# Optimization experiments

Hardware: AMD Instinct MI355X
Metric: run time of the kernel (lower is better)

Reference implementation:

```python
import jax, jax.numpy as jnp
import numpy as np
from jax import lax

S_IN = 16; V_IN = 16; S_OUT = 16; V_OUT = 16
SIZE = 7; STRIDE = 2; PAD = 3; EPS = 1e-5
# n_basis per (rep_out, rep_in) pair = n_radial(3) * number of allowed CG paths
NB = {('s','s'): 3, ('s','v'): 3, ('s','t'): 9, ('v','s'): 3, ('v','v'): 9, ('v','t'): 21}
DIMS = {'s': 1, 'v': 3, 't': 9}  # repr1, repr3, repr3x3 dimensions


def _basis(key, nb, d_out, d_in):
    # Stand-in for the constant steerable basis (spherical harmonics x Clebsch-Gordan
    # x radial windows). These are data-independent constants in se3cnn; the compute
    # pattern (weighted basis sum -> dense 3D conv) is identical.
    return jax.random.normal(key, (nb, d_out, d_in, SIZE, SIZE, SIZE), jnp.float32) / np.sqrt(SIZE ** 3)


def setup_inputs() -> dict:
    key = jax.random.key(0)
    ks = jax.random.split(key, 16)
    inp = {"sv": jax.random.normal(ks[0], (4, S_IN + 3 * V_IN, 32, 32, 32), jnp.float32)}
    mul_in = {'s': S_IN, 'v': V_IN, 't': V_IN}
    i = 1
    for o in ['s', 'v']:
        mo = S_OUT if o == 's' else V_OUT
        for a in ['s', 'v', 't']:
            nb = NB[(o, a)]
            inp[f"basis_{o}{a}"] = _basis(ks[i], nb, DIMS[o], DIMS[a])
            inp[f"w_{o}{a}"] = jax.random.normal(ks[i + 1], (mo, mul_in[a], nb), jnp.float32) / np.sqrt(nb * mul_in[a] * DIMS[a])
            i += 2
    inp["bn_g_s"] = jnp.ones((S_OUT,), jnp.float32)
    inp["bn_g_v"] = jnp.ones((V_OUT,), jnp.float32)
    inp["bias_s"] = jnp.zeros((S_OUT,), jnp.float32)
    return inp


def _block(w, basis):
    # w: [mul_out, mul_in, nb], basis: [nb, d_out, d_in, 7,7,7] -> [mul_out*d_out, mul_in*d_in, 7,7,7]
    mo, mi, nb = w.shape
    do, di = basis.shape[1], basis.shape[2]
    k = jnp.einsum('uvb,bijxyz->uivjxyz', w, basis)
    return k.reshape(mo * do, mi * di, SIZE, SIZE, SIZE)


def _forward(sv, w_ss, w_sv, w_st, w_vs, w_vv, w_vt,
             basis_ss, basis_sv, basis_st, basis_vs, basis_vv, basis_vt,
             bn_g_s, bn_g_v, bias_s):
    B = sv.shape[0]; sp = sv.shape[2:]
    # TensorProduct: vector fields -> vector (x) vector = repr3x3 (9 channels each)
    v = sv[:, S_IN:].reshape(B, V_IN, 3, *sp)
    t = jnp.einsum('buixyz,bujxyz->buijxyz', v, v).reshape(B, V_IN * 9, *sp)
    svt = jnp.concatenate([sv, t], axis=1)  # [B, S_IN + 3*V_IN + 9*V_IN, X,Y,Z]
    # SE3Convolution: assemble kernel from steerable basis, then dense 3D conv
    row_s = jnp.concatenate([_block(w_ss, basis_ss), _block(w_sv, basis_sv), _block(w_st, basis_st)], axis=1)
    row_v = jnp.concatenate([_block(w_vs, basis_vs), _block(w_vv, basis_vv), _block(w_vt, basis_vt)], axis=1)
    kernel = jnp.concatenate([row_s, row_v], axis=0)  # [S_OUT + 3*V_OUT, 208, 7,7,7]
    y = lax.conv_general_dilated(svt, kernel, (STRIDE,) * 3, [(PAD, PAD)] * 3,
                                 dimension_numbers=('NCDHW', 'OIDHW', 'NCDHW'))
    osp = y.shape[2:]
    # SE3BatchNorm: per-field second-moment normalization (training-mode batch stats)
    ys = y[:, :S_OUT]
    yv = y[:, S_OUT:].reshape(B, V_OUT, 3, *osp)
    var_s = jnp.mean(ys * ys, axis=(0, 2, 3, 4))
    ys = ys * (bn_g_s / jnp.sqrt(var_s + EPS))[None, :, None, None, None]
    var_v = jnp.mean(yv * yv, axis=(0, 2, 3, 4, 5))
    yv = yv * (bn_g_v / jnp.sqrt(var_v + EPS))[None, :, None, None, None, None]
    # BiasRelu: bias + relu on scalar fields only; vector fields pass through
    ys = jax.nn.relu(ys + bias_s[None, :, None, None, None])
    return jnp.concatenate([ys, yv.reshape(B, 3 * V_OUT, *osp)], axis=1)


def reference(sv, w_ss, w_sv, w_st, w_vs, w_vv, w_vt,
              basis_ss, basis_sv, basis_st, basis_vs, basis_vv, basis_vt,
              bn_g_s, bn_g_v, bias_s):
    return _forward(sv, w_ss, w_sv, w_st, w_vs, w_vv, w_vt,
                    basis_ss, basis_sv, basis_st, basis_vs, basis_vv, basis_vt,
                    bn_g_s, bn_g_v, bias_s)
```

## Files before the change

kernel.cpp:

```cpp
#include <hip/hip_runtime.h>
#include <hip/hip_bf16.h>


using f4  = __attribute__((ext_vector_type(4)))  float;
using f16v= __attribute__((ext_vector_type(16))) float;
using s8  = __attribute__((ext_vector_type(8)))  short;

#define C_TOT 160
#define PZ_   37
#define NTAP  343
#define NROW  (4 * PZ_ * PZ_)
#define KSN   8
#define SLICE_E 1048576

#define AROW    1232
#define AE_ROWS 19
#define AO_ROWS 18
#define AE_SZ   23552
#define AO_OFF  23552
#define AO_SZ   22528
#define B_OFF   46080
#define BSZ     14336
#define LDS_SZ  (B_OFF + 2 * BSZ)

__device__ __forceinline__ void gl_lds16(const void* g, void* l) {
    __builtin_amdgcn_global_load_lds(
        (const __attribute__((address_space(1))) unsigned int*)g,
        (__attribute__((address_space(3))) unsigned int*)l, 16, 0, 0);
}

__device__ __forceinline__ void pair_ij(int p, int& i, int& j) {
    if (p < 3)      { i = p; j = p; }
    else if (p == 3){ i = 0; j = 1; }
    else if (p == 4){ i = 0; j = 2; }
    else            { i = 1; j = 2; }
}

struct bf2 { __hip_bfloat16 x, y; };
struct bh4 { __hip_bfloat16 x, y, z, w; };

__global__ void prep_kernel(
    const float* __restrict__ sv,
    const float* __restrict__ b_ss, const float* __restrict__ w_ss,
    const float* __restrict__ b_sv, const float* __restrict__ w_sv,
    const float* __restrict__ b_st, const float* __restrict__ w_st,
    const float* __restrict__ b_vs, const float* __restrict__ w_vs,
    const float* __restrict__ b_vv, const float* __restrict__ w_vv,
    const float* __restrict__ b_vt, const float* __restrict__ w_vt,
    __hip_bfloat16* __restrict__ xt, __hip_bfloat16* __restrict__ wl)
{
    __shared__ float S[13056];
    const int tid = threadIdx.x;

    if (blockIdx.x < 1372) {
        float* L = S;
        float* W = S + 768;
        const int tap = blockIdx.x >> 2;
        const int jq  = (blockIdx.x & 3) * 10;
        for (int r = tid; r < 750; r += 256) {
            float v;
            if (r < 3)        v = b_ss[r * NTAP + tap];
            else if (r < 12)  v = b_sv[(r - 3) * NTAP + tap];
            else if (r < 93)  v = b_st[(r - 12) * NTAP + tap];
            else if (r < 102) v = b_vs[(r - 93) * NTAP + tap];
            else if (r < 183) v = b_vv[(r - 102) * NTAP + tap];
            else              v = b_vt[(r - 183) * NTAP + tap];
            L[r] = v;
        }
        for (int r = tid; r < 12288; r += 256) {
            float v;
            if (r < 768)       v = w_ss[r];
            else if (r < 1536) v = w_sv[r - 768];
            else if (r < 3840) v = w_st[r - 1536];
            else if (r < 4608) v = w_vs[r - 3840];
            else if (r < 6912) v = w_vv[r - 4608];
            else               v = w_vt[r - 6912];
            W[r] = v;
        }
        __syncthreads();
        for (int j = jq; j < jq + 10; ++j) {
            const int idx = j * 256 + tid;
            const int c = idx % C_TOT, n = idx / C_TOT;
            float acc = 0.f;
            if (n < 16) {
                const int u = n;
                if (c < 16) {
                    for (int t = 0; t < 3; ++t) acc += W[(u*16 + c)*3 + t] * L[t];
                } else if (c < 64) {
                    int mm = (c-16)/3, di = (c-16)%3;
                    for (int t = 0; t < 3; ++t)
                        acc += W[768 + (u*16+mm)*3 + t] * L[3 + t*3 + di];
                } else {
                    int q = c-64, mm = q/6, p = q%6, i, jj;
                    pair_ij(p, i, jj);
                    int d1 = i*3+jj, d2 = jj*3+i;
                    for (int t = 0; t < 9; ++t) {
                        float bs = L[12 + t*9 + d1];
                        if (i != jj) bs += L[12 + t*9 + d2];
                        acc += W[1536 + (u*16+mm)*9 + t] * bs;
                    }
                }
            } else {
                const int u = (n-16)/3, dn = (n-16)%3;
                if (c < 16) {
                    for (int t = 0; t < 3; ++t)
                        acc += W[3840 + (u*16+c)*3 + t] * L[93 + t*3 + dn];
                } else if (c < 64) {
                    int mm = (c-16)/3, di = (c-16)%3;
                    for (int t = 0; t < 9; ++t)
                        acc += W[4608 + (u*16+mm)*9 + t] * L[102 + (t*3+dn)*3 + di];
                } else {
                    int q = c-64, mm = q/6, p = q%6, i, jj;
                    pair_ij(p, i, jj);
                    int d1 = i*3+jj, d2 = jj*3+i;
                    for (int t = 0; t < 21; ++t) {
                        float bs = L[183 + (t*3+dn)*9 + d1];
                        if (i != jj) bs += L[183 + (t*3+dn)*9 + d2];
                        acc += W[6912 + (u*16+mm)*21 + t] * bs;
                    }
                }
            }
            const int chunk = c >> 4, cw = c & 15;
            wl[((size_t)chunk * NTAP + tap) * 1024 + (size_t)n * 16 + cw] =
                __float2bfloat16(acc);
        }
    } else {
        float* row = S;
        const int bid = blockIdx.x - 1372;
        const int y = bid % 37, z = (bid / 37) % 37, b = bid / 1369;
        const bool interior = (z >= 3 && z < 35 && y >= 3 && y < 35);
        if (interior) {
            const float* src = sv + (size_t)b * 2097152 + (z-3) * 1024 + (y-3) * 32;
            for (int f = tid; f < 2048; f += 256) {
                int ch = f >> 5, x = f & 31;
                row[x * 66 + ch] = src[(size_t)ch * 32768 + x];
            }
        }
        __syncthreads();
        for (int e2 = tid; e2 < 38 * 80; e2 += 256) {
            const int s = e2 / 80, cp = e2 % 80, c = cp * 2;
            float v0 = 0.f, v1 = 0.f;
            if (interior && s >= 3 && s < 35) {
                const int x = s - 3;
                if (c < 64) {
                    v0 = row[x * 66 + c];
                    v1 = row[x * 66 + c + 1];
                } else {
                    int q = c - 64, u = q / 6, p = q % 6, i, j;
                    pair_ij(p, i, j);
                    v0 = row[x * 66 + 16 + u * 3 + i] * row[x * 66 + 16 + u * 3 + j];
                    pair_ij(p + 1, i, j);
                    v1 = row[x * 66 + 16 + u * 3 + i] * row[x * 66 + 16 + u * 3 + j];
                }
            }
            bf2 w{__float2bfloat16(v0), __float2bfloat16(v1)};
            const int chunk = c >> 4, cw = c & 15;
            *(bf2*)(xt + ((size_t)chunk * NROW + bid) * 608 + s * 16 + cw) = w;
        }
    }
}

__global__ __launch_bounds__(256, 2) void conv_mfma_kernel(
    const __hip_bfloat16* __restrict__ xt,
    const __hip_bfloat16* __restrict__ wl,
    __hip_bfloat16* __restrict__ y4b)
{
    __shared__ __align__(16) char lds[LDS_SZ];

    const int phys = blockIdx.x;
    const int bid  = (phys & 7) * (64 * KSN / 8) + (phys >> 3);

    const int low3 = bid & 7;
    const int rest = bid >> 3;
    const int ks   = rest % KSN;
    const int mb   = (rest / KSN) * 8 + low3;
    const int b    = mb >> 4;
    const int oz   = mb & 15;

    const int tid  = threadIdx.x;
    const int w    = tid >> 6;
    const int lane = tid & 63;
    const int m    = lane & 31;
    const int h    = lane >> 5;

    int invAE[6]; int nAE = 0;
#pragma unroll
    for (int k = 0; k < 6; ++k) {
        const int i = w + 4 * k;
        if (i < 23) {
            const int o = i * 1024 + lane * 16;
            int r = o / AROW;
            int rem = o - r * AROW;
            if (r > AE_ROWS - 1) { r = AE_ROWS - 1; rem = 0; }
            if (rem >= 1216) rem = 0;
            const int s  = rem >> 5;
            const int cg = ((rem >> 4) & 1) ^ ((s >> 1) & 1);
            invAE[k] = (2 * r) * 608 + s * 16 + cg * 8;
            nAE = k + 1;
        }
    }
    int invAO[6]; int nAO = 0;
#pragma unroll
    for (int k = 0; k < 6; ++k) {
        const int i = w + 4 * k;
        if (i < 22) {
            const int o = i * 1024 + lane * 16;
            int r = o / AROW;
            int rem = o - r * AROW;
            if (r > AO_ROWS - 1) { r = AO_ROWS - 1; rem = 0; }
            if (rem >= 1216) rem = 0;
            const int s  = rem >> 5;
            const int cg = ((rem >> 4) & 1) ^ ((s >> 1) & 1);
            invAO[k] = (2 * r + 1) * 608 + s * 16 + cg * 8;
            nAO = k + 1;
        }
    }
    int invB[4]; int nB = 0;
#pragma unroll
    for (int k = 0; k < 4; ++k) {
        const int i = w + 4 * k;
        if (i < 14) {
            const int kx = i >> 1, nt = i & 1;
            invB[k] = kx * 1024 + (nt * 32 + m) * 16 + h * 8;
            nB = k + 1;
        }
    }

    f16v acc[2][2];
    for (int t = 0; t < 2; ++t)
        for (int n = 0; n < 2; ++n)
            for (int k = 0; k < 16; ++k) acc[t][n][k] = 0.f;

    const int rA0   = ((m >> 4) << 2) + ((m >> 2) & 3);
    const int sbase = (w << 3) + ((m & 3) << 1);

    auto stageAE = [&](int g) {
        const int chunk = g / 7, kz = g - chunk * 7;
        const size_t u = ((size_t)chunk * NROW + (size_t)(b * PZ_ + 2 * oz + kz) * PZ_) * 608;
#pragma unroll
        for (int k = 0; k < 6; ++k)
            if (k < nAE) gl_lds16(xt + u + invAE[k], lds + (w + 4 * k) * 1024);
    };
    auto stageAO = [&](int g) {
        const int chunk = g / 7, kz = g - chunk * 7;
        const size_t u = ((size_t)chunk * NROW + (size_t)(b * PZ_ + 2 * oz + kz) * PZ_) * 608;
#pragma unroll
        for (int k = 0; k < 6; ++k)
            if (k < nAO) gl_lds16(xt + u + invAO[k], lds + AO_OFF + (w + 4 * k) * 1024);
    };
    auto stageB = [&](int g, int kyv, int bsel) {
        const int chunk = g / 7, kz = g - chunk * 7;
        const size_t u = ((size_t)chunk * NTAP + (size_t)(kz * 7 + kyv) * 7) * 1024;
        char* dst = lds + B_OFF + bsel * BSZ;
#pragma unroll
        for (int k = 0; k < 4; ++k)
            if (k < nB) gl_lds16(wl + u + invB[k], dst + (w + 4 * k) * 1024);
    };

    auto compute = [&](int ky, int bsel) {
        const int abase = (ky & 1) ? AO_OFF : 0;
        const char* abp = lds + abase + (rA0 + (ky >> 1)) * AROW;
        const char* bbp = lds + B_OFF + bsel * BSZ;
#pragma unroll
        for (int kx = 0; kx < 7; ++kx) {
            const int s   = sbase + kx;
            const int cgp = h ^ ((s >> 1) & 1);
            const char* ap = abp + s * 32 + cgp * 16;
            const s8 a0 = *(const s8*)(ap);
            const s8 a1 = *(const s8*)(ap + 8 * AROW);
            const char* bp = bbp + kx * 2048 + h * 512 + m * 16;
            const s8 b0 = *(const s8*)(bp);
            const s8 b1 = *(const s8*)(bp + 1024);
            acc[0][0] = __builtin_amdgcn_mfma_f32_32x32x16_bf16(a0, b0, acc[0][0], 0, 0, 0);
            acc[0][1] = __builtin_amdgcn_mfma_f32_32x32x16_bf16(a0, b1, acc[0][1], 0, 0, 0);
            acc[1][0] = __builtin_amdgcn_mfma_f32_32x32x16_bf16(a1, b0, acc[1][0], 0, 0, 0);
            acc[1][1] = __builtin_amdgcn_mfma_f32_32x32x16_bf16(a1, b1, acc[1][1], 0, 0, 0);
        }
    };

    const int G = (ks < 6) ? 9 : 8;
    const int T = G * 7;
    stageAO(ks);
    stageB(ks, 1, 0);
    __syncthreads();
    int bB = 0;
    for (int t = 0; t < T; ++t) {
        const int gi = t / 7, p = t - gi * 7;
        const int g  = ks + gi * KSN;
        const int ky = (p < 3) ? (2 * p + 1) : (2 * (p - 3));
        const int tn = t + 1;
        if (tn < T) {
            const int gin = tn / 7, pn = tn - gin * 7;
            const int kyn = (pn < 3) ? (2 * pn + 1) : (2 * (pn - 3));
            stageB(ks + gin * KSN, kyn, bB ^ 1);
        }
        if (p == 0) stageAE(g);
        else if (p == 3 && g + KSN < 70) stageAO(g + KSN);
        compute(ky, bB);
        __syncthreads();
        bB ^= 1;
    }

    const int nl = lane & 31;
    f4* yb = (f4*)lds;
    __hip_bfloat16* dst0 = y4b + (size_t)ks * SLICE_E + (size_t)(b * 64) * 4096
                         + (size_t)oz * 256;
#pragma unroll
    for (int t = 0; t < 2; ++t) {
        __syncthreads();
#pragma unroll
        for (int nt = 0; nt < 2; ++nt) {
            const int n = nt * 32 + nl;
#pragma unroll
            for (int q = 0; q < 4; ++q) {
                const int rr = 2 * q + h;
                f4 v = { acc[t][nt][4*q], acc[t][nt][4*q+1],
                         acc[t][nt][4*q+2], acc[t][nt][4*q+3] };
                yb[n * 33 + rr * 4 + w] = v;
            }
        }
        __syncthreads();
        for (int j = tid; j < 2048; j += 256) {
            const int n  = j >> 5, sp = j & 31;
            f4 v = yb[n * 33 + sp];
            const int rr = sp >> 2, wq = sp & 3;
            const int yo = t * 8 + (rr >> 2) * 4 + (rr & 3);
            bh4 p{__float2bfloat16(v.x), __float2bfloat16(v.y),
                  __float2bfloat16(v.z), __float2bfloat16(v.w)};
            *(bh4*)(dst0 + (size_t)n * 4096 + yo * 16 + wq * 4) = p;
        }
    }
}

__global__ void combine_reduce_kernel(const __hip_bfloat16* __restrict__ y4b,
                                      float* __restrict__ yc,
                                      float* __restrict__ sums2)
{
    const int n = blockIdx.x & 63, q = blockIdx.x >> 6;
    const size_t base = ((size_t)q * 64 + n) * 4096;
    float s = 0.f;
    for (int i = threadIdx.x; i < 1024; i += 256) {
        const size_t off = base + (size_t)i * 4;
        f4 v = {0.f, 0.f, 0.f, 0.f};
#pragma unroll
        for (int k = 0; k < KSN; ++k) {
            bh4 r = *(const bh4*)(y4b + off + (size_t)k * SLICE_E);
            v.x += (float)r.x; v.y += (float)r.y;
            v.z += (float)r.z; v.w += (float)r.w;
        }
        *(f4*)(yc + off) = v;
        s += v.x * v.x + v.y * v.y + v.z * v.z + v.w * v.w;
    }
    __shared__ float red[256];
    red[threadIdx.x] = s;
    __syncthreads();
    for (int st = 128; st > 0; st >>= 1) {
        if (threadIdx.x < st) red[threadIdx.x] += red[threadIdx.x + st];
        __syncthreads();
    }
    if (threadIdx.x == 0) sums2[n * 4 + q] = red[0];
}

__global__ void finalize_kernel(const float* __restrict__ yc,
                                const float* __restrict__ sums2,
                                const float* __restrict__ g_s,
                                const float* __restrict__ g_v,
                                const float* __restrict__ bias_s,
                                float* __restrict__ out)
{
    const int idx = blockIdx.x * 256 + threadIdx.x;
    const int n = (idx >> 12) & 63;
    float v = yc[idx];
    if (n < 16) {
        float sum = sums2[n*4] + sums2[n*4+1] + sums2[n*4+2] + sums2[n*4+3];
        float var = sum * (1.0f / 16384.0f);
        float sc  = g_s[n] / sqrtf(var + 1e-5f);
        v = fmaxf(v * sc + bias_s[n], 0.f);
    } else {
        int u = (n - 16) / 3;
        float sum = 0.f;
        for (int k = 0; k < 12; ++k) sum += sums2[(16 + u * 3) * 4 + k];
        float var = sum * (1.0f / 49152.0f);
        v = v * (g_v[u] / sqrtf(var + 1e-5f));
    }
    out[idx] = v;
}

extern "C" void kernel_launch(void* const* d_in, const int* in_sizes, int n_in,
                              void* d_out, int out_size, void* d_ws, size_t ws_size,
                              hipStream_t stream)
{
    const float* sv    = (const float*)d_in[0];
    const float* b_ss  = (const float*)d_in[1];
    const float* w_ss  = (const float*)d_in[2];
    const float* b_sv  = (const float*)d_in[3];
    const float* w_sv  = (const float*)d_in[4];
    const float* b_st  = (const float*)d_in[5];
    const float* w_st  = (const float*)d_in[6];
    const float* b_vs  = (const float*)d_in[7];
    const float* w_vs  = (const float*)d_in[8];
    const float* b_vv  = (const float*)d_in[9];
    const float* w_vv  = (const float*)d_in[10];
    const float* b_vt  = (const float*)d_in[11];
    const float* w_vt  = (const float*)d_in[12];
    const float* bn_gs = (const float*)d_in[13];
    const float* bn_gv = (const float*)d_in[14];
    const float* bias_s= (const float*)d_in[15];
    float* out = (float*)d_out;

    char* ws = (char*)d_ws;
    constexpr size_t XT_BYTES = (size_t)10 * NROW * 1216;
    constexpr size_t WL_BYTES = (size_t)10 * NTAP * 2048;
    constexpr size_t Y4_BYTES = (size_t)KSN * SLICE_E * 2;
    constexpr size_t YC_BYTES = (size_t)4 * 64 * 4096 * 4;

    __hip_bfloat16* xt  = (__hip_bfloat16*)ws;
    __hip_bfloat16* wl  = (__hip_bfloat16*)(ws + XT_BYTES);
    __hip_bfloat16* y4b = (__hip_bfloat16*)(ws + XT_BYTES + WL_BYTES);
    float* yc    = (float*)(ws + XT_BYTES + WL_BYTES + Y4_BYTES);
    float* sums2 = (float*)(ws + XT_BYTES + WL_BYTES + Y4_BYTES + YC_BYTES);

    prep_kernel<<<1372 + 5476, 256, 0, stream>>>(
        sv, b_ss, w_ss, b_sv, w_sv, b_st, w_st, b_vs, w_vs, b_vv, w_vv,
        b_vt, w_vt, xt, wl);
    conv_mfma_kernel<<<64 * KSN, 256, 0, stream>>>(xt, wl, y4b);
    combine_reduce_kernel<<<256, 256, 0, stream>>>(y4b, yc, sums2);
    finalize_kernel<<<4096, 256, 0, stream>>>(yc, sums2, bn_gs, bn_gv, bias_s, out);
}
```

Before: 275.4 us.

## Compute two output z-slices per conv block to reuse staged weight tiles

Each conv workgroup now handles two adjacent output depth slices instead of one. It stages two A stripes in LDS and reuses every B (weight) tile across both, doubling the MFMA work per B load. This halves the grid to 256 blocks and drops occupancy to one block per CU, since LDS grows to about 120KB and there are twice as many accumulators. The aim is to cut redundant weight traffic into LDS. The cost is fewer waves to hide latency and a risk of spilling accumulator registers.

```diff
diff --git a/kernel.cpp b/kernel.cpp
--- a/kernel.cpp
+++ b/kernel.cpp
@@ -11,17 +11,17 @@
 #define NTAP  343
 #define NROW  (4 * PZ_ * PZ_)
 #define KSN   8
+#define GRID_C 256
 #define SLICE_E 1048576
 
-#define AROW    1232
-#define AE_ROWS 19
-#define AO_ROWS 18
-#define AE_SZ   23552
-#define AO_OFF  23552
-#define AO_SZ   22528
-#define B_OFF   46080
-#define BSZ     14336
-#define LDS_SZ  (B_OFF + 2 * BSZ)
+#define AROW      1232
+#define AE_ROWS   19
+#define AO_ROWS   18
+#define AO_OFF    23552
+#define STRIPE_SZ 46080
+#define B_OFF     92160
+#define BSZ       14336
+#define LDS_SZ    (B_OFF + 2 * BSZ)
 
 __device__ __forceinline__ void gl_lds16(const void* g, void* l) {
     __builtin_amdgcn_global_load_lds(
@@ -160,7 +160,7 @@
     }
 }
 
-__global__ __launch_bounds__(256, 2) void conv_mfma_kernel(
+__global__ __launch_bounds__(256, 1) void conv_mfma_kernel(
     const __hip_bfloat16* __restrict__ xt,
     const __hip_bfloat16* __restrict__ wl,
     __hip_bfloat16* __restrict__ y4b)
@@ -168,14 +168,14 @@
     __shared__ __align__(16) char lds[LDS_SZ];
 
     const int phys = blockIdx.x;
-    const int bid  = (phys & 7) * (64 * KSN / 8) + (phys >> 3);
+    const int bid  = (phys & 7) * (GRID_C / 8) + (phys >> 3);
 
     const int low3 = bid & 7;
     const int rest = bid >> 3;
     const int ks   = rest % KSN;
     const int mb   = (rest / KSN) * 8 + low3;
-    const int b    = mb >> 4;
-    const int oz   = mb & 15;
+    const int b    = mb >> 3;
+    const int ozp  = mb & 7;
 
     const int tid  = threadIdx.x;
     const int w    = tid >> 6;
@@ -226,27 +226,33 @@
         }
     }
 
-    f16v acc[2][2];
-    for (int t = 0; t < 2; ++t)
+    f16v acc[4][2];
+#pragma unroll
+    for (int t = 0; t < 4; ++t)
+#pragma unroll
         for (int n = 0; n < 2; ++n)
             for (int k = 0; k < 16; ++k) acc[t][n][k] = 0.f;
 
     const int rA0   = ((m >> 4) << 2) + ((m >> 2) & 3);
     const int sbase = (w << 3) + ((m & 3) << 1);
 
-    auto stageAE = [&](int g) {
+    auto stageAE = [&](int g, int st) {
         const int chunk = g / 7, kz = g - chunk * 7;
-        const size_t u = ((size_t)chunk * NROW + (size_t)(b * PZ_ + 2 * oz + kz) * PZ_) * 608;
+        const size_t u = ((size_t)chunk * NROW
+                        + (size_t)(b * PZ_ + 4 * ozp + 2 * st + kz) * PZ_) * 608;
+        char* base = lds + st * STRIPE_SZ;
 #pragma unroll
         for (int k = 0; k < 6; ++k)
-            if (k < nAE) gl_lds16(xt + u + invAE[k], lds + (w + 4 * k) * 1024);
+            if (k < nAE) gl_lds16(xt + u + invAE[k], base + (w + 4 * k) * 1024);
     };
-    auto stageAO = [&](int g) {
+    auto stageAO = [&](int g, int st) {
         const int chunk = g / 7, kz = g - chunk * 7;
-        const size_t u = ((size_t)chunk * NROW + (size_t)(b * PZ_ + 2 * oz + kz) * PZ_) * 608;
+        const size_t u = ((size_t)chunk * NROW
+                        + (size_t)(b * PZ_ + 4 * ozp + 2 * st + kz) * PZ_) * 608;
+        char* base = lds + st * STRIPE_SZ + AO_OFF;
 #pragma unroll
         for (int k = 0; k < 6; ++k)
-            if (k < nAO) gl_lds16(xt + u + invAO[k], lds + AO_OFF + (w + 4 * k) * 1024);
+            if (k < nAO) gl_lds16(xt + u + invAO[k], base + (w + 4 * k) * 1024);
     };
     auto stageB = [&](int g, int kyv, int bsel) {
         const int chunk = g / 7, kz = g - chunk * 7;
@@ -258,8 +264,8 @@
     };
 
     auto compute = [&](int ky, int bsel) {
-        const int abase = (ky & 1) ? AO_OFF : 0;
-        const char* abp = lds + abase + (rA0 + (ky >> 1)) * AROW;
+        const int pb = (ky & 1) ? AO_OFF : 0;
+        const char* abp = lds + pb + (rA0 + (ky >> 1)) * AROW;
         const char* bbp = lds + B_OFF + bsel * BSZ;
 #pragma unroll
         for (int kx = 0; kx < 7; ++kx) {
@@ -268,6 +274,8 @@
             const char* ap = abp + s * 32 + cgp * 16;
             const s8 a0 = *(const s8*)(ap);
             const s8 a1 = *(const s8*)(ap + 8 * AROW);
+            const s8 a2 = *(const s8*)(ap + STRIPE_SZ);
+            const s8 a3 = *(const s8*)(ap + STRIPE_SZ + 8 * AROW);
             const char* bp = bbp + kx * 2048 + h * 512 + m * 16;
             const s8 b0 = *(const s8*)(bp);
             const s8 b1 = *(const s8*)(bp + 1024);
@@ -275,12 +283,17 @@
             acc[0][1] = __builtin_amdgcn_mfma_f32_32x32x16_bf16(a0, b1, acc[0][1], 0, 0, 0);
             acc[1][0] = __builtin_amdgcn_mfma_f32_32x32x16_bf16(a1, b0, acc[1][0], 0, 0, 0);
             acc[1][1] = __builtin_amdgcn_mfma_f32_32x32x16_bf16(a1, b1, acc[1][1], 0, 0, 0);
+            acc[2][0] = __builtin_amdgcn_mfma_f32_32x32x16_bf16(a2, b0, acc[2][0], 0, 0, 0);
+            acc[2][1] = __builtin_amdgcn_mfma_f32_32x32x16_bf16(a2, b1, acc[2][1], 0, 0, 0);
+            acc[3][0] = __builtin_amdgcn_mfma_f32_32x32x16_bf16(a3, b0, acc[3][0], 0, 0, 0);
+            acc[3][1] = __builtin_amdgcn_mfma_f32_32x32x16_bf16(a3, b1, acc[3][1], 0, 0, 0);
         }
     };
 
-    const int G = (ks < 6) ? 9 : 8;
+    const int G = (70 - ks + KSN - 1) / KSN;
     const int T = G * 7;
-    stageAO(ks);
+    stageAO(ks, 0);
+    stageAO(ks, 1);
     stageB(ks, 1, 0);
     __syncthreads();
     int bB = 0;
@@ -294,8 +307,10 @@
             const int kyn = (pn < 3) ? (2 * pn + 1) : (2 * (pn - 3));
             stageB(ks + gin * KSN, kyn, bB ^ 1);
         }
-        if (p == 0) stageAE(g);
-        else if (p == 3 && g + KSN < 70) stageAO(g + KSN);
+        if      (p == 0) stageAE(g, 0);
+        else if (p == 1) stageAE(g, 1);
+        else if (p == 3 && g + KSN < 70) stageAO(g + KSN, 0);
+        else if (p == 4 && g + KSN < 70) stageAO(g + KSN, 1);
         compute(ky, bB);
         __syncthreads();
         bB ^= 1;
@@ -304,9 +319,10 @@
     const int nl = lane & 31;
     f4* yb = (f4*)lds;
     __hip_bfloat16* dst0 = y4b + (size_t)ks * SLICE_E + (size_t)(b * 64) * 4096
-                         + (size_t)oz * 256;
-#pragma unroll
-    for (int t = 0; t < 2; ++t) {
+                         + (size_t)(2 * ozp) * 256;
+#pragma unroll
+    for (int e = 0; e < 4; ++e) {
+        const int zi = e >> 1, tt = e & 1;
         __syncthreads();
 #pragma unroll
         for (int nt = 0; nt < 2; ++nt) {
@@ -314,8 +330,8 @@
 #pragma unroll
             for (int q = 0; q < 4; ++q) {
                 const int rr = 2 * q + h;
-                f4 v = { acc[t][nt][4*q], acc[t][nt][4*q+1],
-                         acc[t][nt][4*q+2], acc[t][nt][4*q+3] };
+                f4 v = { acc[e][nt][4*q], acc[e][nt][4*q+1],
+                         acc[e][nt][4*q+2], acc[e][nt][4*q+3] };
                 yb[n * 33 + rr * 4 + w] = v;
             }
         }
@@ -324,10 +340,10 @@
             const int n  = j >> 5, sp = j & 31;
             f4 v = yb[n * 33 + sp];
             const int rr = sp >> 2, wq = sp & 3;
-            const int yo = t * 8 + (rr >> 2) * 4 + (rr & 3);
+            const int yo = tt * 8 + (rr >> 2) * 4 + (rr & 3);
             bh4 p{__float2bfloat16(v.x), __float2bfloat16(v.y),
                   __float2bfloat16(v.z), __float2bfloat16(v.w)};
-            *(bh4*)(dst0 + (size_t)n * 4096 + yo * 16 + wq * 4) = p;
+            *(bh4*)(dst0 + (size_t)n * 4096 + zi * 256 + yo * 16 + wq * 4) = p;
         }
     }
 }
@@ -423,7 +439,7 @@
     prep_kernel<<<1372 + 5476, 256, 0, stream>>>(
         sv, b_ss, w_ss, b_sv, w_sv, b_st, w_st, b_vs, w_vs, b_vv, w_vv,
         b_vt, w_vt, xt, wl);
-    conv_mfma_kernel<<<64 * KSN, 256, 0, stream>>>(xt, wl, y4b);
+    conv_mfma_kernel<<<GRID_C, 256, 0, stream>>>(xt, wl, y4b);
     combine_reduce_kernel<<<256, 256, 0, stream>>>(y4b, yc, sums2);
     finalize_kernel<<<4096, 256, 0, stream>>>(yc, sums2, bn_gs, bn_gv, bias_s, out);
 }
```

Result: no change. 272.8 us (-1.0%).

## Load weight tiles straight into registers instead of staging through LDS

Applied to the files above, without the earlier changes.

Drops the double-buffered LDS staging of the B (weight) operand. Each lane now loads its MFMA B fragments directly from global memory into two register sets (Ba/Bb), one prefetched a step ahead. With the weight buffers gone, barriers are needed only when the A tiles are restaged (every third or fourth step), not every iteration, and the LDS footprint shrinks. The cost is 28 extra vector registers per lane, which may hurt occupancy under launch_bounds(256,2), and exposed global-load latency if the one-step prefetch is too short.

```diff
diff --git a/kernel.cpp b/kernel.cpp
--- a/kernel.cpp
+++ b/kernel.cpp
@@ -16,12 +16,8 @@
 #define AROW    1232
 #define AE_ROWS 19
 #define AO_ROWS 18
-#define AE_SZ   23552
 #define AO_OFF  23552
-#define AO_SZ   22528
-#define B_OFF   46080
-#define BSZ     14336
-#define LDS_SZ  (B_OFF + 2 * BSZ)
+#define LDS_SZ  46080
 
 __device__ __forceinline__ void gl_lds16(const void* g, void* l) {
     __builtin_amdgcn_global_load_lds(
@@ -160,6 +156,35 @@
     }
 }
 
+
+#define LOADB(B_, g_, ky_) do {                                               \
+    const int ch_ = (g_) / 7, kz_ = (g_) - ch_ * 7;                           \
+    const __hip_bfloat16* wb_ = wlb                                           \
+        + ((size_t)ch_ * NTAP + (size_t)(kz_ * 7 + (ky_)) * 7) * 1024;        \
+    _Pragma("unroll")                                                         \
+    for (int kx_ = 0; kx_ < 7; ++kx_) {                                       \
+        B_[2*kx_]   = *(const s8*)(wb_ + kx_ * 1024);                         \
+        B_[2*kx_+1] = *(const s8*)(wb_ + kx_ * 1024 + 512);                   \
+    }                                                                         \
+} while (0)
+
+#define COMPT(B_, ky_) do {                                                   \
+    const char* abp_ = lds + (((ky_) & 1) ? AO_OFF : 0)                       \
+                     + (rA0 + ((ky_) >> 1)) * AROW;                           \
+    _Pragma("unroll")                                                         \
+    for (int kx_ = 0; kx_ < 7; ++kx_) {                                       \
+        const int s_   = sbase + kx_;                                         \
+        const int cgp_ = h ^ ((s_ >> 1) & 1);                                 \
+        const char* ap_ = abp_ + s_ * 32 + cgp_ * 16;                         \
+        const s8 a0_ = *(const s8*)(ap_);                                     \
+        const s8 a1_ = *(const s8*)(ap_ + 8 * AROW);                          \
+        acc[0][0] = __builtin_amdgcn_mfma_f32_32x32x16_bf16(a0_, B_[2*kx_],   acc[0][0], 0, 0, 0); \
+        acc[0][1] = __builtin_amdgcn_mfma_f32_32x32x16_bf16(a0_, B_[2*kx_+1], acc[0][1], 0, 0, 0); \
+        acc[1][0] = __builtin_amdgcn_mfma_f32_32x32x16_bf16(a1_, B_[2*kx_],   acc[1][0], 0, 0, 0); \
+        acc[1][1] = __builtin_amdgcn_mfma_f32_32x32x16_bf16(a1_, B_[2*kx_+1], acc[1][1], 0, 0, 0); \
+    }                                                                         \
+} while (0)
+
 __global__ __launch_bounds__(256, 2) void conv_mfma_kernel(
     const __hip_bfloat16* __restrict__ xt,
     const __hip_bfloat16* __restrict__ wl,
@@ -215,16 +240,8 @@
             nAO = k + 1;
         }
     }
-    int invB[4]; int nB = 0;
-#pragma unroll
-    for (int k = 0; k < 4; ++k) {
-        const int i = w + 4 * k;
-        if (i < 14) {
-            const int kx = i >> 1, nt = i & 1;
-            invB[k] = kx * 1024 + (nt * 32 + m) * 16 + h * 8;
-            nB = k + 1;
-        }
-    }
+
+    const __hip_bfloat16* wlb = wl + (size_t)(m * 16 + h * 8);
 
     f16v acc[2][2];
     for (int t = 0; t < 2; ++t)
@@ -236,75 +253,54 @@
 
     auto stageAE = [&](int g) {
         const int chunk = g / 7, kz = g - chunk * 7;
-        const size_t u = ((size_t)chunk * NROW + (size_t)(b * PZ_ + 2 * oz + kz) * PZ_) * 608;
+        const size_t u = ((size_t)chunk * NROW
+                        + (size_t)(b * PZ_ + 2 * oz + kz) * PZ_) * 608;
 #pragma unroll
         for (int k = 0; k < 6; ++k)
             if (k < nAE) gl_lds16(xt + u + invAE[k], lds + (w + 4 * k) * 1024);
     };
     auto stageAO = [&](int g) {
         const int chunk = g / 7, kz = g - chunk * 7;
-        const size_t u = ((size_t)chunk * NROW + (size_t)(b * PZ_ + 2 * oz + kz) * PZ_) * 608;
+        const size_t u = ((size_t)chunk * NROW
+                        + (size_t)(b * PZ_ + 2 * oz + kz) * PZ_) * 608;
 #pragma unroll
         for (int k = 0; k < 6; ++k)
             if (k < nAO) gl_lds16(xt + u + invAO[k], lds + AO_OFF + (w + 4 * k) * 1024);
     };
-    auto stageB = [&](int g, int kyv, int bsel) {
-        const int chunk = g / 7, kz = g - chunk * 7;
-        const size_t u = ((size_t)chunk * NTAP + (size_t)(kz * 7 + kyv) * 7) * 1024;
-        char* dst = lds + B_OFF + bsel * BSZ;
-#pragma unroll
-        for (int k = 0; k < 4; ++k)
-            if (k < nB) gl_lds16(wl + u + invB[k], dst + (w + 4 * k) * 1024);
-    };
-
-    auto compute = [&](int ky, int bsel) {
-        const int abase = (ky & 1) ? AO_OFF : 0;
-        const char* abp = lds + abase + (rA0 + (ky >> 1)) * AROW;
-        const char* bbp = lds + B_OFF + bsel * BSZ;
-#pragma unroll
-        for (int kx = 0; kx < 7; ++kx) {
-            const int s   = sbase + kx;
-            const int cgp = h ^ ((s >> 1) & 1);
-            const char* ap = abp + s * 32 + cgp * 16;
-            const s8 a0 = *(const s8*)(ap);
-            const s8 a1 = *(const s8*)(ap + 8 * AROW);
-            const char* bp = bbp + kx * 2048 + h * 512 + m * 16;
-            const s8 b0 = *(const s8*)(bp);
-            const s8 b1 = *(const s8*)(bp + 1024);
-            acc[0][0] = __builtin_amdgcn_mfma_f32_32x32x16_bf16(a0, b0, acc[0][0], 0, 0, 0);
-            acc[0][1] = __builtin_amdgcn_mfma_f32_32x32x16_bf16(a0, b1, acc[0][1], 0, 0, 0);
-            acc[1][0] = __builtin_amdgcn_mfma_f32_32x32x16_bf16(a1, b0, acc[1][0], 0, 0, 0);
-            acc[1][1] = __builtin_amdgcn_mfma_f32_32x32x16_bf16(a1, b1, acc[1][1], 0, 0, 0);
-        }
-    };
-
-    const int G = (ks < 6) ? 9 : 8;
+
+    const int G = (70 - ks + KSN - 1) / KSN;
     const int T = G * 7;
+    s8 Ba[14], Bb[14];
     stageAO(ks);
-    stageB(ks, 1, 0);
-    __syncthreads();
-    int bB = 0;
+    LOADB(Ba, ks, 1);
+    bool useA = true;
     for (int t = 0; t < T; ++t) {
         const int gi = t / 7, p = t - gi * 7;
         const int g  = ks + gi * KSN;
+        if (p == 0)      { __syncthreads(); stageAE(g); }
+        else if (p == 3) { __syncthreads(); if (g + KSN < 70) stageAO(g + KSN); }
         const int ky = (p < 3) ? (2 * p + 1) : (2 * (p - 3));
         const int tn = t + 1;
-        if (tn < T) {
+        int gn = 0, kyn = 0;
+        const bool hasN = (tn < T);
+        if (hasN) {
             const int gin = tn / 7, pn = tn - gin * 7;
-            const int kyn = (pn < 3) ? (2 * pn + 1) : (2 * (pn - 3));
-            stageB(ks + gin * KSN, kyn, bB ^ 1);
-        }
-        if (p == 0) stageAE(g);
-        else if (p == 3 && g + KSN < 70) stageAO(g + KSN);
-        compute(ky, bB);
-        __syncthreads();
-        bB ^= 1;
+            gn  = ks + gin * KSN;
+            kyn = (pn < 3) ? (2 * pn + 1) : (2 * (pn - 3));
+        }
+        if (useA) {
+            if (hasN) LOADB(Bb, gn, kyn);
+            COMPT(Ba, ky);
+        } else {
+            if (hasN) LOADB(Ba, gn, kyn);
+            COMPT(Bb, ky);
+        }
+        useA = !useA;
     }
 
     const int nl = lane & 31;
     f4* yb = (f4*)lds;
-    __hip_bfloat16* dst0 = y4b + (size_t)ks * SLICE_E + (size_t)(b * 64) * 4096
-                         + (size_t)oz * 256;
+    __hip_bfloat16* dst0 = y4b + (size_t)ks * SLICE_E + (size_t)(b * 64) * 4096;
 #pragma unroll
     for (int t = 0; t < 2; ++t) {
         __syncthreads();
@@ -327,7 +323,7 @@
             const int yo = t * 8 + (rr >> 2) * 4 + (rr & 3);
             bh4 p{__float2bfloat16(v.x), __float2bfloat16(v.y),
                   __float2bfloat16(v.z), __float2bfloat16(v.w)};
-            *(bh4*)(dst0 + (size_t)n * 4096 + yo * 16 + wq * 4) = p;
+            *(bh4*)(dst0 + (size_t)n * 4096 + oz * 256 + yo * 16 + wq * 4) = p;
         }
     }
 }
```

Result: slower. 560.7 us (+103.6%).
